# Kernel optimization log

Hardware: AMD Instinct MI355X
Metric: run time of the kernel (lower is better)

The kernel has to match this reference:

```python
import jax, jax.numpy as jnp
import numpy as np

DIM = 512
NUM_HEADS = 8
HEAD_DIM = DIM // NUM_HEADS
MAX_FRAMES = 64
EPS = 1e-5


def setup_inputs() -> dict:
    key = jax.random.key(0)
    ks = jax.random.split(key, 6)
    x = jax.random.normal(ks[0], (4, DIM, 16, 32, 32), dtype=jnp.float32)
    W_qkv = jax.random.normal(ks[1], (3 * DIM, DIM), dtype=jnp.float32) * (DIM ** -0.5)
    W_proj = jax.random.normal(ks[2], (DIM, DIM), dtype=jnp.float32) * (DIM ** -0.5)
    b_proj = jnp.zeros((DIM,), dtype=jnp.float32)
    rel_bias = jax.random.normal(ks[3], (MAX_FRAMES, MAX_FRAMES), dtype=jnp.float32) * 0.02
    ln_g = jnp.ones((DIM,), dtype=jnp.float32)
    ln_b = jnp.zeros((DIM,), dtype=jnp.float32)
    return {"x": x, "W_qkv": W_qkv, "W_proj": W_proj, "b_proj": b_proj,
            "rel_bias": rel_bias, "ln_g": ln_g, "ln_b": ln_b}


def reference(x, W_qkv, W_proj, b_proj, rel_bias, ln_g, ln_b):
    B, C, F, H, W = x.shape
    h = NUM_HEADS
    scale = HEAD_DIM ** -0.5
    # (B,C,F,H,W) -> (B*H*W, F, C)
    xr = jnp.transpose(x, (0, 3, 4, 2, 1)).reshape(B * H * W, F, C)
    residual = xr
    # LayerNorm over channel dim
    mu = jnp.mean(xr, axis=-1, keepdims=True)
    var = jnp.mean(jnp.square(xr - mu), axis=-1, keepdims=True)
    xn = (xr - mu) * jax.lax.rsqrt(var + EPS) * ln_g + ln_b
    # QKV projection (torch Linear: x @ W.T)
    qkv = xn @ W_qkv.T  # (BHW, F, 3C)
    q, k, v = jnp.split(qkv, 3, axis=-1)
    split_heads = lambda t: t.reshape(t.shape[0], F, h, HEAD_DIM).transpose(0, 2, 1, 3)
    q, k, v = split_heads(q), split_heads(k), split_heads(v)  # (BHW, h, F, d)
    attn = jnp.einsum('bhid,bhjd->bhij', q, k) * scale + rel_bias[:F, :F]
    attn = jax.nn.softmax(attn, axis=-1)
    out = jnp.einsum('bhij,bhjd->bhid', attn, v)  # (BHW, h, F, d)
    out = out.transpose(0, 2, 1, 3).reshape(B * H * W, F, C)
    out = out @ W_proj.T + b_proj + residual
    # (B*H*W, F, C) -> (B, C, F, H, W)
    out = out.reshape(B, H, W, F, C).transpose(0, 4, 3, 1, 2)
    return out
```

## Files before the change

### kernel.cpp

```cpp
#include <hip/hip_runtime.h>

typedef unsigned short ushort_t;
typedef __attribute__((ext_vector_type(4))) float f32x4;
typedef __attribute__((ext_vector_type(8))) short s16x8;
typedef __attribute__((ext_vector_type(4))) short s16x4;

#define SB 8388608
#define SC 16384
#define SF 1024

static __device__ __forceinline__ float bf2f(ushort_t u) {
    union { float f; unsigned int i; } x; x.i = ((unsigned int)u) << 16; return x.f;
}
static __device__ __forceinline__ ushort_t f2bf(float f) {
    union { float f; unsigned int i; } x; x.f = f;
    unsigned int u = x.i;
    unsigned int r = (u + 0x7FFFu + ((u >> 16) & 1u)) >> 16;
    return (ushort_t)r;
}

static __device__ __forceinline__ void gload16(const void* g, void* l) {
    __builtin_amdgcn_global_load_lds(
        (const __attribute__((address_space(1))) unsigned int*)g,
        (__attribute__((address_space(3))) unsigned int*)l, 16, 0, 0);
}

static __device__ __forceinline__ void wg_barrier() {
    asm volatile("" ::: "memory");
    __builtin_amdgcn_s_barrier();
    asm volatile("" ::: "memory");
}

__global__ void k_cvt(const float* __restrict__ a, int n1,
                      const float* __restrict__ b, int n2,
                      ushort_t* __restrict__ o1, ushort_t* __restrict__ o2) {
    int i = blockIdx.x * blockDim.x + threadIdx.x;
    if (i < n1) o1[i] = f2bf(a[i]);
    if (i < n2) o2[i] = f2bf(b[i]);
}

__global__ __launch_bounds__(256) void k_ln_transpose(
        const float* __restrict__ x, const float* __restrict__ g,
        const float* __restrict__ bta, ushort_t* __restrict__ xn) {
    __shared__ float tile[32 * 513];
    __shared__ float gg[512];
    __shared__ float bb[512];
    int bid = blockIdx.x;
    int b = bid >> 9;
    int f = (bid >> 5) & 15;
    int h = bid & 31;
    int t = threadIdx.x;
    for (int c = t; c < 512; c += 256) { gg[c] = g[c]; bb[c] = bta[c]; }
    const float* xp = x + (size_t)b * SB + (size_t)f * SF + h * 32;
    int wq4 = (t & 7) * 4;
    int c0 = t >> 3;
    for (int it = 0; it < 16; ++it) {
        int c = c0 + it * 32;
        f32x4 v = *(const f32x4*)(xp + (size_t)c * SC + wq4);
        tile[(wq4 + 0) * 513 + c] = v[0];
        tile[(wq4 + 1) * 513 + c] = v[1];
        tile[(wq4 + 2) * 513 + c] = v[2];
        tile[(wq4 + 3) * 513 + c] = v[3];
    }
    __syncthreads();
    int lane = t & 63;
    int wave = t >> 6;
    for (int wi = 0; wi < 8; ++wi) {
        int ww = wave * 8 + wi;
        float s = 0.f, s2 = 0.f;
        #pragma unroll
        for (int j = 0; j < 8; ++j) {
            float v = tile[ww * 513 + lane + j * 64];
            s += v; s2 += v * v;
        }
        #pragma unroll
        for (int off = 32; off; off >>= 1) { s += __shfl_xor(s, off); s2 += __shfl_xor(s2, off); }
        float mean = s * (1.f / 512.f);
        float var = s2 * (1.f / 512.f) - mean * mean;
        float rstd = rsqrtf(var + 1e-5f);
        size_t row = ((size_t)((b * 32 + h) * 32 + ww)) * 16 + f;
        ushort_t* op = xn + row * 512 + lane * 8;
        union { ushort_t a[8]; s16x8 v; } u;
        #pragma unroll
        for (int j = 0; j < 8; ++j) {
            int c = lane * 8 + j;
            float v = tile[ww * 513 + c];
            u.a[j] = f2bf((v - mean) * rstd * gg[c] + bb[c]);
        }
        *(s16x8*)op = u.v;
    }
}

__global__ __launch_bounds__(512) void k_qkv_attn(
        const ushort_t* __restrict__ xn, const ushort_t* __restrict__ wq,
        const float* __restrict__ rb, ushort_t* __restrict__ att) {
    __shared__ __align__(16) char U[122880];
    ushort_t* qsm = (ushort_t*)(U);
    ushort_t* ksm = (ushort_t*)(U + 16384);
    ushort_t* vT  = (ushort_t*)(U + 32768);

    const int t = threadIdx.x;
    const int lane = t & 63;
    const int wv = t >> 6;
    const int l16 = lane & 15;
    const int lg = lane >> 4;
    const int m0 = blockIdx.x * 128;
    const int wm = wv >> 2;
    const int wn = wv & 3;
    ushort_t* psw = ksm + wv * 1024;
    ushort_t* olw = qsm + wv * 1024;

    auto stageA = [&](int buf, int kb) {
        ushort_t* dst = (ushort_t*)(U + buf * 16384);
        #pragma unroll
        for (int it = 0; it < 2; ++it) {
            int f = t + it * 512;
            int row = f >> 3, slot = f & 7;
            const ushort_t* src = xn + (size_t)(m0 + row) * 512 + kb * 64 + ((slot ^ (row & 7)) << 3);
            gload16(src, dst + f * 8);
        }
    };
    auto stageB = [&](int buf, int kb, int h) {
        ushort_t* dst = (ushort_t*)(U + 49152 + buf * 24576);
        #pragma unroll
        for (int it = 0; it < 3; ++it) {
            int f = t + it * 512;
            int brow = f >> 3, slot = f & 7;
            int wrow = (brow >> 6) * 512 + h * 64 + (brow & 63);
            const ushort_t* src = wq + (size_t)wrow * 512 + kb * 64 + ((slot ^ (brow & 7)) << 3);
            gload16(src, dst + f * 8);
        }
    };

    for (int h = 0; h < 8; ++h) {
        __syncthreads();
        stageA(0, 0); stageB(0, 0, h);
        stageA(1, 1); stageB(1, 1, h);

        f32x4 acc[4][3];
        #pragma unroll
        for (int a1 = 0; a1 < 4; ++a1)
            #pragma unroll
            for (int a2 = 0; a2 < 3; ++a2)
                acc[a1][a2] = (f32x4){0.f, 0.f, 0.f, 0.f};

        for (int kb = 0; kb < 8; ++kb) {
            int cur = kb % 3;
            if (kb < 6) {
                stageA((kb + 2) % 3, kb + 2);
                stageB((kb + 2) % 3, kb + 2, h);
                asm volatile("s_waitcnt vmcnt(10)" ::: "memory");
            } else if (kb == 6) {
                asm volatile("s_waitcnt vmcnt(5)" ::: "memory");
            } else {
                asm volatile("s_waitcnt vmcnt(0)" ::: "memory");
            }
            wg_barrier();
            const ushort_t* Ac = (const ushort_t*)(U + cur * 16384);
            const ushort_t* Bc = (const ushort_t*)(U + 49152 + cur * 24576);
            #pragma unroll
            for (int kk = 0; kk < 2; ++kk) {
                int koff = kk * 64 + lg * 16;
                s16x8 af[4], bf[3];
                #pragma unroll
                for (int mf = 0; mf < 4; ++mf) {
                    int row = wm * 64 + mf * 16 + l16;
                    af[mf] = *(const s16x8*)&Ac[row * 64 + ((koff ^ ((row & 7) << 4)) >> 1)];
                }
                #pragma unroll
                for (int nf = 0; nf < 3; ++nf) {
                    int nrow = wn * 48 + nf * 16 + l16;
                    bf[nf] = *(const s16x8*)&Bc[nrow * 64 + ((koff ^ ((nrow & 7) << 4)) >> 1)];
                }
                #pragma unroll
                for (int mf = 0; mf < 4; ++mf)
                    #pragma unroll
                    for (int nf = 0; nf < 3; ++nf)
                        acc[mf][nf] = __builtin_amdgcn_mfma_f32_16x16x32_bf16(af[mf], bf[nf], acc[mf][nf], 0, 0, 0);
            }
            wg_barrier();
        }

        #pragma unroll
        for (int mf = 0; mf < 4; ++mf) {
            int mbase = wm * 64 + mf * 16 + lg * 4;
            #pragma unroll
            for (int nf = 0; nf < 3; ++nf) {
                int nn = wn * 48 + nf * 16 + l16;
                int seg = nn >> 6;
                int d = nn & 63;
                if (seg == 2) {
                    union { s16x4 v; ushort_t a[4]; } pk;
                    #pragma unroll
                    for (int r = 0; r < 4; ++r) pk.a[r] = f2bf(acc[mf][nf][r]);
                    *(s16x4*)&vT[d * 136 + mbase] = pk.v;
                } else {
                    ushort_t* dst = seg ? ksm : qsm;
                    #pragma unroll
                    for (int r = 0; r < 4; ++r) {
                        int m = mbase + r;
                        dst[m * 64 + (d ^ ((m & 7) << 3))] = f2bf(acc[mf][nf][r]);
                    }
                }
            }
        }
        __syncthreads();

        {
            int arow = wv * 16 + l16;
            int sw = (arow & 7) << 4;
            f32x4 sacc = (f32x4){0.f, 0.f, 0.f, 0.f};
            #pragma unroll
            for (int kk = 0; kk < 2; ++kk) {
                int off = kk * 64 + lg * 16;
                s16x8 ka = *(const s16x8*)&ksm[arow * 64 + ((off ^ sw) >> 1)];
                s16x8 qb = *(const s16x8*)&qsm[arow * 64 + ((off ^ sw) >> 1)];
                sacc = __builtin_amdgcn_mfma_f32_16x16x32_bf16(ka, qb, sacc, 0, 0, 0);
            }
            const float* rbp = rb + l16 * 64 + lg * 4;
            float p[4];
            float mx = -1e30f;
            #pragma unroll
            for (int r = 0; r < 4; ++r) {
                p[r] = sacc[r] * 0.125f + rbp[r];
                mx = fmaxf(mx, p[r]);
            }
            mx = fmaxf(mx, __shfl_xor(mx, 16));
            mx = fmaxf(mx, __shfl_xor(mx, 32));
            float sum = 0.f;
            #pragma unroll
            for (int r = 0; r < 4; ++r) { p[r] = __expf(p[r] - mx); sum += p[r]; }
            sum += __shfl_xor(sum, 16);
            sum += __shfl_xor(sum, 32);
            float inv = 1.f / sum;
            {
                union { s16x4 v; ushort_t a[4]; } pk;
                #pragma unroll
                for (int r = 0; r < 4; ++r) pk.a[r] = f2bf(p[r] * inv);
                *(s16x4*)&psw[l16 * 16 + lg * 4] = pk.v;
            }
            asm volatile("s_waitcnt lgkmcnt(0)" ::: "memory");
            s16x8 ap = (s16x8){0, 0, 0, 0, 0, 0, 0, 0};
            if (lg < 2) ap = *(const s16x8*)&psw[l16 * 16 + lg * 8];
            int jj = (lg < 2) ? lg * 8 : 0;
            f32x4 ov[4];
            #pragma unroll
            for (int ff = 0; ff < 4; ++ff) {
                int d = ff * 16 + l16;
                s16x8 bv = *(const s16x8*)&vT[d * 136 + wv * 16 + jj];
                ov[ff] = __builtin_amdgcn_mfma_f32_16x16x32_bf16(ap, bv, (f32x4){0.f, 0.f, 0.f, 0.f}, 0, 0, 0);
            }
            #pragma unroll
            for (int ff = 0; ff < 4; ++ff)
                #pragma unroll
                for (int r = 0; r < 4; ++r)
                    olw[(lg * 4 + r) * 64 + ff * 16 + l16] = f2bf(ov[ff][r]);
            asm volatile("s_waitcnt lgkmcnt(0)" ::: "memory");
            {
                int i2 = lane >> 2;
                int c2 = (lane & 3) * 16;
                s16x8 w0 = *(const s16x8*)&olw[i2 * 64 + c2];
                s16x8 w1 = *(const s16x8*)&olw[i2 * 64 + c2 + 8];
                ushort_t* op = att + (size_t)(m0 + wv * 16 + i2) * 512 + h * 64 + c2;
                *(s16x8*)op = w0;
                *(s16x8*)(op + 8) = w1;
            }
        }
    }
}

__global__ __launch_bounds__(512) void k_proj_out(
        const ushort_t* __restrict__ att, const ushort_t* __restrict__ wp,
        const float* __restrict__ bp, const float* __restrict__ x,
        float* __restrict__ out) {
    __shared__ __align__(16) char U[73728];
    int bid = blockIdx.x;
    int nh = bid & 1;
    int fq = (bid >> 1) & 3;
    int h = (bid >> 3) & 31;
    int b = bid >> 8;
    const int n0 = nh * 256;
    const int t = threadIdx.x;
    const int lane = t & 63;
    const int wv = t >> 6;
    const int l16 = lane & 15;
    const int lg = lane >> 4;
    const int wm = wv >> 2;
    const int wn = wv & 3;
    size_t attbase = ((size_t)(b * 32 + h) * 32) * 16 + fq * 4;

    auto stA = [&](int buf, int ks) {
        int row = t >> 2, slot = t & 3;
        int w = row & 31, fl = row >> 5;
        const ushort_t* src = att + (attbase + (size_t)w * 16 + fl) * 512 + ks * 32 + ((slot ^ ((row >> 2) & 3)) << 3);
        gload16(src, (ushort_t*)(U + buf * 8192) + t * 8);
    };
    auto stB = [&](int buf, int ks) {
        #pragma unroll
        for (int i = 0; i < 2; ++i) {
            int u = t + i * 512;
            int row = u >> 2, slot = u & 3;
            const ushort_t* src = wp + (size_t)(n0 + row) * 512 + ks * 32 + ((slot ^ ((row >> 2) & 3)) << 3);
            gload16(src, (ushort_t*)(U + 24576 + buf * 16384) + u * 8);
        }
    };

    f32x4 acc[4][4];
    #pragma unroll
    for (int m = 0; m < 4; ++m)
        #pragma unroll
        for (int n = 0; n < 4; ++n)
            acc[m][n] = (f32x4){0.f, 0.f, 0.f, 0.f};

    stA(0, 0); stB(0, 0);
    stA(1, 1); stB(1, 1);
    for (int ks = 0; ks < 16; ++ks) {
        int cur = ks % 3;
        if (ks < 14) {
            stA((ks + 2) % 3, ks + 2);
            stB((ks + 2) % 3, ks + 2);
            asm volatile("s_waitcnt vmcnt(6)" ::: "memory");
        } else if (ks == 14) {
            asm volatile("s_waitcnt vmcnt(3)" ::: "memory");
        } else {
            asm volatile("s_waitcnt vmcnt(0)" ::: "memory");
        }
        wg_barrier();
        s16x8 af[4], bf[4];
        #pragma unroll
        for (int mf = 0; mf < 4; ++mf) {
            int row = wm * 64 + mf * 16 + l16;
            af[mf] = *(const s16x8*)((ushort_t*)(U + cur * 8192) + row * 32 + ((lg ^ ((row >> 2) & 3)) << 3));
        }
        #pragma unroll
        for (int nf = 0; nf < 4; ++nf) {
            int nrow = wn * 64 + nf * 16 + l16;
            bf[nf] = *(const s16x8*)((ushort_t*)(U + 24576 + cur * 16384) + nrow * 32 + ((lg ^ ((nrow >> 2) & 3)) << 3));
        }
        #pragma unroll
        for (int mf = 0; mf < 4; ++mf)
            #pragma unroll
            for (int nf = 0; nf < 4; ++nf)
                acc[mf][nf] = __builtin_amdgcn_mfma_f32_16x16x32_bf16(bf[nf], af[mf], acc[mf][nf], 0, 0, 0);
        wg_barrier();
    }

    size_t obase = (size_t)b * SB + (size_t)(fq * 4) * SF + h * 32;
    #pragma unroll
    for (int mf = 0; mf < 4; ++mf) {
        int m = wm * 64 + mf * 16 + l16;
        int w = m & 31, fl = m >> 5;
        size_t base_m = obase + (size_t)fl * SF + w;
        #pragma unroll
        for (int nf = 0; nf < 4; ++nf) {
            int col0 = n0 + wn * 64 + nf * 16 + lg * 4;
            #pragma unroll
            for (int r = 0; r < 4; ++r) {
                int col = col0 + r;
                size_t a = base_m + (size_t)col * SC;
                out[a] = acc[mf][nf][r] + bp[col] + x[a];
            }
        }
    }
}

extern "C" void kernel_launch(void* const* d_in, const int* in_sizes, int n_in,
                              void* d_out, int out_size, void* d_ws, size_t ws_size,
                              hipStream_t stream) {
    const float* x     = (const float*)d_in[0];
    const float* wqkv  = (const float*)d_in[1];
    const float* wproj = (const float*)d_in[2];
    const float* bproj = (const float*)d_in[3];
    const float* rb    = (const float*)d_in[4];
    const float* lng   = (const float*)d_in[5];
    const float* lnb   = (const float*)d_in[6];
    float* out = (float*)d_out;
    char* ws = (char*)d_ws;
    ushort_t* xn   = (ushort_t*)(ws);
    ushort_t* att  = (ushort_t*)(ws + 67108864);
    ushort_t* wq16 = (ushort_t*)(ws + 134217728);
    ushort_t* wp16 = (ushort_t*)(ws + 135790592);

    k_cvt<<<3072, 256, 0, stream>>>(wqkv, 1536 * 512, wproj, 512 * 512, wq16, wp16);
    k_ln_transpose<<<2048, 256, 0, stream>>>(x, lng, lnb, xn);
    k_qkv_attn<<<512, 512, 0, stream>>>(xn, wq16, rb, att);
    k_proj_out<<<1024, 512, 0, stream>>>(att, wp16, bproj, x, out);
}
```

Before: 320.3 us.

## Process two heads per QKV GEMM pass with double-buffered staging

The fused QKV+attention kernel now computes Q/K/V for two heads at once, a 384-wide N tile per pass. This halves how often the activation A-tile is reloaded and halves the number of head-loop iterations and barriers. The staging pipeline goes from triple to double buffering to fit the larger B tile, and each wave's accumulator count doubles to 24 f32x4 fragments. This raises register pressure and LDS use to 128KB, and the shallower prefetch may expose more global-load latency.

```diff
diff --git a/kernel.cpp b/kernel.cpp
--- a/kernel.cpp
+++ b/kernel.cpp
@@ -94,10 +94,7 @@
 __global__ __launch_bounds__(512) void k_qkv_attn(
         const ushort_t* __restrict__ xn, const ushort_t* __restrict__ wq,
         const float* __restrict__ rb, ushort_t* __restrict__ att) {
-    __shared__ __align__(16) char U[122880];
-    ushort_t* qsm = (ushort_t*)(U);
-    ushort_t* ksm = (ushort_t*)(U + 16384);
-    ushort_t* vT  = (ushort_t*)(U + 32768);
+    __shared__ __align__(16) char U[131072];
 
     const int t = threadIdx.x;
     const int lane = t & 63;
@@ -107,8 +104,8 @@
     const int m0 = blockIdx.x * 128;
     const int wm = wv >> 2;
     const int wn = wv & 3;
-    ushort_t* psw = ksm + wv * 1024;
-    ushort_t* olw = qsm + wv * 1024;
+    ushort_t* psw = (ushort_t*)(U + 100352) + wv * 256;
+    ushort_t* olw = (ushort_t*)(U + 104448) + wv * 1024;
 
     auto stageA = [&](int buf, int kb) {
         ushort_t* dst = (ushort_t*)(U + buf * 16384);
@@ -120,62 +117,62 @@
             gload16(src, dst + f * 8);
         }
     };
-    auto stageB = [&](int buf, int kb, int h) {
-        ushort_t* dst = (ushort_t*)(U + 49152 + buf * 24576);
-        #pragma unroll
-        for (int it = 0; it < 3; ++it) {
+    auto stageB = [&](int buf, int kb, int hp) {
+        ushort_t* dst = (ushort_t*)(U + 32768 + buf * 49152);
+        #pragma unroll
+        for (int it = 0; it < 6; ++it) {
             int f = t + it * 512;
             int brow = f >> 3, slot = f & 7;
-            int wrow = (brow >> 6) * 512 + h * 64 + (brow & 63);
+            int seg = brow >> 7;
+            int hh = (brow >> 6) & 1;
+            int d = brow & 63;
+            int wrow = seg * 512 + (hp * 2 + hh) * 64 + d;
             const ushort_t* src = wq + (size_t)wrow * 512 + kb * 64 + ((slot ^ (brow & 7)) << 3);
             gload16(src, dst + f * 8);
         }
     };
 
-    for (int h = 0; h < 8; ++h) {
+    for (int hp = 0; hp < 4; ++hp) {
         __syncthreads();
-        stageA(0, 0); stageB(0, 0, h);
-        stageA(1, 1); stageB(1, 1, h);
-
-        f32x4 acc[4][3];
+        stageA(0, 0); stageB(0, 0, hp);
+
+        f32x4 acc[4][6];
         #pragma unroll
         for (int a1 = 0; a1 < 4; ++a1)
             #pragma unroll
-            for (int a2 = 0; a2 < 3; ++a2)
+            for (int a2 = 0; a2 < 6; ++a2)
                 acc[a1][a2] = (f32x4){0.f, 0.f, 0.f, 0.f};
 
         for (int kb = 0; kb < 8; ++kb) {
-            int cur = kb % 3;
-            if (kb < 6) {
-                stageA((kb + 2) % 3, kb + 2);
-                stageB((kb + 2) % 3, kb + 2, h);
-                asm volatile("s_waitcnt vmcnt(10)" ::: "memory");
-            } else if (kb == 6) {
-                asm volatile("s_waitcnt vmcnt(5)" ::: "memory");
+            int cur = kb & 1;
+            if (kb < 7) {
+                stageA(cur ^ 1, kb + 1);
+                stageB(cur ^ 1, kb + 1, hp);
+                asm volatile("s_waitcnt vmcnt(8)" ::: "memory");
             } else {
                 asm volatile("s_waitcnt vmcnt(0)" ::: "memory");
             }
             wg_barrier();
             const ushort_t* Ac = (const ushort_t*)(U + cur * 16384);
-            const ushort_t* Bc = (const ushort_t*)(U + 49152 + cur * 24576);
+            const ushort_t* Bc = (const ushort_t*)(U + 32768 + cur * 49152);
             #pragma unroll
             for (int kk = 0; kk < 2; ++kk) {
                 int koff = kk * 64 + lg * 16;
-                s16x8 af[4], bf[3];
+                s16x8 af[4], bf[6];
                 #pragma unroll
                 for (int mf = 0; mf < 4; ++mf) {
                     int row = wm * 64 + mf * 16 + l16;
                     af[mf] = *(const s16x8*)&Ac[row * 64 + ((koff ^ ((row & 7) << 4)) >> 1)];
                 }
                 #pragma unroll
-                for (int nf = 0; nf < 3; ++nf) {
-                    int nrow = wn * 48 + nf * 16 + l16;
+                for (int nf = 0; nf < 6; ++nf) {
+                    int nrow = wn * 96 + nf * 16 + l16;
                     bf[nf] = *(const s16x8*)&Bc[nrow * 64 + ((koff ^ ((nrow & 7) << 4)) >> 1)];
                 }
                 #pragma unroll
                 for (int mf = 0; mf < 4; ++mf)
                     #pragma unroll
-                    for (int nf = 0; nf < 3; ++nf)
+                    for (int nf = 0; nf < 6; ++nf)
                         acc[mf][nf] = __builtin_amdgcn_mfma_f32_16x16x32_bf16(af[mf], bf[nf], acc[mf][nf], 0, 0, 0);
             }
             wg_barrier();
@@ -185,17 +182,19 @@
         for (int mf = 0; mf < 4; ++mf) {
             int mbase = wm * 64 + mf * 16 + lg * 4;
             #pragma unroll
-            for (int nf = 0; nf < 3; ++nf) {
-                int nn = wn * 48 + nf * 16 + l16;
-                int seg = nn >> 6;
+            for (int nf = 0; nf < 6; ++nf) {
+                int nn = wn * 96 + nf * 16 + l16;
+                int seg = nn >> 7;
+                int hh = (nn >> 6) & 1;
                 int d = nn & 63;
                 if (seg == 2) {
+                    ushort_t* vTh = (ushort_t*)(U + 65536 + hh * 17408);
                     union { s16x4 v; ushort_t a[4]; } pk;
                     #pragma unroll
                     for (int r = 0; r < 4; ++r) pk.a[r] = f2bf(acc[mf][nf][r]);
-                    *(s16x4*)&vT[d * 136 + mbase] = pk.v;
+                    *(s16x4*)&vTh[d * 136 + mbase] = pk.v;
                 } else {
-                    ushort_t* dst = seg ? ksm : qsm;
+                    ushort_t* dst = (ushort_t*)(U + (seg ? 32768 : 0) + hh * 16384);
                     #pragma unroll
                     for (int r = 0; r < 4; ++r) {
                         int m = mbase + r;
@@ -206,15 +205,20 @@
         }
         __syncthreads();
 
-        {
+        #pragma unroll
+        for (int pp = 0; pp < 2; ++pp) {
+            const ushort_t* qsmP = (const ushort_t*)(U + pp * 16384);
+            const ushort_t* ksmP = (const ushort_t*)(U + 32768 + pp * 16384);
+            const ushort_t* vTP  = (const ushort_t*)(U + 65536 + pp * 17408);
+            int hd = hp * 2 + pp;
             int arow = wv * 16 + l16;
             int sw = (arow & 7) << 4;
             f32x4 sacc = (f32x4){0.f, 0.f, 0.f, 0.f};
             #pragma unroll
             for (int kk = 0; kk < 2; ++kk) {
                 int off = kk * 64 + lg * 16;
-                s16x8 ka = *(const s16x8*)&ksm[arow * 64 + ((off ^ sw) >> 1)];
-                s16x8 qb = *(const s16x8*)&qsm[arow * 64 + ((off ^ sw) >> 1)];
+                s16x8 ka = *(const s16x8*)&ksmP[arow * 64 + ((off ^ sw) >> 1)];
+                s16x8 qb = *(const s16x8*)&qsmP[arow * 64 + ((off ^ sw) >> 1)];
                 sacc = __builtin_amdgcn_mfma_f32_16x16x32_bf16(ka, qb, sacc, 0, 0, 0);
             }
             const float* rbp = rb + l16 * 64 + lg * 4;
@@ -247,7 +251,7 @@
             #pragma unroll
             for (int ff = 0; ff < 4; ++ff) {
                 int d = ff * 16 + l16;
-                s16x8 bv = *(const s16x8*)&vT[d * 136 + wv * 16 + jj];
+                s16x8 bv = *(const s16x8*)&vTP[d * 136 + wv * 16 + jj];
                 ov[ff] = __builtin_amdgcn_mfma_f32_16x16x32_bf16(ap, bv, (f32x4){0.f, 0.f, 0.f, 0.f}, 0, 0, 0);
             }
             #pragma unroll
@@ -261,7 +265,7 @@
                 int c2 = (lane & 3) * 16;
                 s16x8 w0 = *(const s16x8*)&olw[i2 * 64 + c2];
                 s16x8 w1 = *(const s16x8*)&olw[i2 * 64 + c2 + 8];
-                ushort_t* op = att + (size_t)(m0 + wv * 16 + i2) * 512 + h * 64 + c2;
+                ushort_t* op = att + (size_t)(m0 + wv * 16 + i2) * 512 + hd * 64 + c2;
                 *(s16x8*)op = w0;
                 *(s16x8*)(op + 8) = w1;
             }
```

After: 490.1 us. 1.53x slower.

## Shrink QKV-attention blocks to 64 rows with 256 threads for two blocks per CU

Applied to the files above, without the earlier changes.

The fused QKV-projection and attention kernel now processes 64 rows per block with 4 waves instead of 128 rows with 8 waves. Each wave covers all 64 rows against its own 48-column slice of the head's q/k/v weights. The triple-buffered global-to-LDS pipeline with explicit vmcnt waits becomes a double buffer guarded by plain __syncthreads, and the LDS footprint drops to 64KB so two blocks can share a CU. The intent is better latency hiding across blocks, but the weight tiles are now reloaded for half as many rows, and the full barriers likely wait on the just-issued prefetch, which removes much of the load/compute overlap. k_proj_out also gets a min-blocks-per-CU launch bound.

```diff
diff --git a/kernel.cpp b/kernel.cpp
--- a/kernel.cpp
+++ b/kernel.cpp
@@ -91,42 +91,41 @@
     }
 }
 
-__global__ __launch_bounds__(512) void k_qkv_attn(
+__global__ __launch_bounds__(256, 2) void k_qkv_attn(
         const ushort_t* __restrict__ xn, const ushort_t* __restrict__ wq,
         const float* __restrict__ rb, ushort_t* __restrict__ att) {
-    __shared__ __align__(16) char U[122880];
-    ushort_t* qsm = (ushort_t*)(U);
-    ushort_t* ksm = (ushort_t*)(U + 16384);
-    ushort_t* vT  = (ushort_t*)(U + 32768);
+    __shared__ __align__(16) char U[65536];
 
     const int t = threadIdx.x;
     const int lane = t & 63;
     const int wv = t >> 6;
     const int l16 = lane & 15;
     const int lg = lane >> 4;
-    const int m0 = blockIdx.x * 128;
-    const int wm = wv >> 2;
-    const int wn = wv & 3;
-    ushort_t* psw = ksm + wv * 1024;
-    ushort_t* olw = qsm + wv * 1024;
+    const int m0 = blockIdx.x * 64;
+    ushort_t* qsm = (ushort_t*)(U);
+    ushort_t* ksm = (ushort_t*)(U + 8192);
+    ushort_t* vT  = (ushort_t*)(U + 16384);
+    ushort_t* psw = (ushort_t*)(U + 25600) + wv * 256;
+    ushort_t* olw = (ushort_t*)(U + 27648) + wv * 1024;
 
     auto stageA = [&](int buf, int kb) {
-        ushort_t* dst = (ushort_t*)(U + buf * 16384);
+        ushort_t* dst = (ushort_t*)(U + buf * 8192);
         #pragma unroll
         for (int it = 0; it < 2; ++it) {
-            int f = t + it * 512;
+            int f = t + it * 256;
             int row = f >> 3, slot = f & 7;
             const ushort_t* src = xn + (size_t)(m0 + row) * 512 + kb * 64 + ((slot ^ (row & 7)) << 3);
             gload16(src, dst + f * 8);
         }
     };
     auto stageB = [&](int buf, int kb, int h) {
-        ushort_t* dst = (ushort_t*)(U + 49152 + buf * 24576);
-        #pragma unroll
-        for (int it = 0; it < 3; ++it) {
-            int f = t + it * 512;
+        ushort_t* dst = (ushort_t*)(U + 16384 + buf * 24576);
+        #pragma unroll
+        for (int it = 0; it < 6; ++it) {
+            int f = t + it * 256;
             int brow = f >> 3, slot = f & 7;
-            int wrow = (brow >> 6) * 512 + h * 64 + (brow & 63);
+            int seg = brow >> 6;
+            int wrow = seg * 512 + h * 64 + (brow & 63);
             const ushort_t* src = wq + (size_t)wrow * 512 + kb * 64 + ((slot ^ (brow & 7)) << 3);
             gload16(src, dst + f * 8);
         }
@@ -135,7 +134,6 @@
     for (int h = 0; h < 8; ++h) {
         __syncthreads();
         stageA(0, 0); stageB(0, 0, h);
-        stageA(1, 1); stageB(1, 1, h);
 
         f32x4 acc[4][3];
         #pragma unroll
@@ -145,31 +143,23 @@
                 acc[a1][a2] = (f32x4){0.f, 0.f, 0.f, 0.f};
 
         for (int kb = 0; kb < 8; ++kb) {
-            int cur = kb % 3;
-            if (kb < 6) {
-                stageA((kb + 2) % 3, kb + 2);
-                stageB((kb + 2) % 3, kb + 2, h);
-                asm volatile("s_waitcnt vmcnt(10)" ::: "memory");
-            } else if (kb == 6) {
-                asm volatile("s_waitcnt vmcnt(5)" ::: "memory");
-            } else {
-                asm volatile("s_waitcnt vmcnt(0)" ::: "memory");
-            }
-            wg_barrier();
-            const ushort_t* Ac = (const ushort_t*)(U + cur * 16384);
-            const ushort_t* Bc = (const ushort_t*)(U + 49152 + cur * 24576);
+            int cur = kb & 1;
+            if (kb < 7) { stageA(cur ^ 1, kb + 1); stageB(cur ^ 1, kb + 1, h); }
+            __syncthreads();
+            const ushort_t* Ac = (const ushort_t*)(U + cur * 8192);
+            const ushort_t* Bc = (const ushort_t*)(U + 16384 + cur * 24576);
             #pragma unroll
             for (int kk = 0; kk < 2; ++kk) {
                 int koff = kk * 64 + lg * 16;
                 s16x8 af[4], bf[3];
                 #pragma unroll
                 for (int mf = 0; mf < 4; ++mf) {
-                    int row = wm * 64 + mf * 16 + l16;
+                    int row = mf * 16 + l16;
                     af[mf] = *(const s16x8*)&Ac[row * 64 + ((koff ^ ((row & 7) << 4)) >> 1)];
                 }
                 #pragma unroll
                 for (int nf = 0; nf < 3; ++nf) {
-                    int nrow = wn * 48 + nf * 16 + l16;
+                    int nrow = wv * 48 + nf * 16 + l16;
                     bf[nf] = *(const s16x8*)&Bc[nrow * 64 + ((koff ^ ((nrow & 7) << 4)) >> 1)];
                 }
                 #pragma unroll
@@ -178,22 +168,22 @@
                     for (int nf = 0; nf < 3; ++nf)
                         acc[mf][nf] = __builtin_amdgcn_mfma_f32_16x16x32_bf16(af[mf], bf[nf], acc[mf][nf], 0, 0, 0);
             }
-            wg_barrier();
+            __syncthreads();
         }
 
         #pragma unroll
         for (int mf = 0; mf < 4; ++mf) {
-            int mbase = wm * 64 + mf * 16 + lg * 4;
+            int mbase = mf * 16 + lg * 4;
             #pragma unroll
             for (int nf = 0; nf < 3; ++nf) {
-                int nn = wn * 48 + nf * 16 + l16;
+                int nn = wv * 48 + nf * 16 + l16;
                 int seg = nn >> 6;
                 int d = nn & 63;
                 if (seg == 2) {
                     union { s16x4 v; ushort_t a[4]; } pk;
                     #pragma unroll
                     for (int r = 0; r < 4; ++r) pk.a[r] = f2bf(acc[mf][nf][r]);
-                    *(s16x4*)&vT[d * 136 + mbase] = pk.v;
+                    *(s16x4*)&vT[d * 72 + mbase] = pk.v;
                 } else {
                     ushort_t* dst = seg ? ksm : qsm;
                     #pragma unroll
@@ -239,7 +229,7 @@
                 for (int r = 0; r < 4; ++r) pk.a[r] = f2bf(p[r] * inv);
                 *(s16x4*)&psw[l16 * 16 + lg * 4] = pk.v;
             }
-            asm volatile("s_waitcnt lgkmcnt(0)" ::: "memory");
+            __syncthreads();
             s16x8 ap = (s16x8){0, 0, 0, 0, 0, 0, 0, 0};
             if (lg < 2) ap = *(const s16x8*)&psw[l16 * 16 + lg * 8];
             int jj = (lg < 2) ? lg * 8 : 0;
@@ -247,7 +237,7 @@
             #pragma unroll
             for (int ff = 0; ff < 4; ++ff) {
                 int d = ff * 16 + l16;
-                s16x8 bv = *(const s16x8*)&vT[d * 136 + wv * 16 + jj];
+                s16x8 bv = *(const s16x8*)&vT[d * 72 + wv * 16 + jj];
                 ov[ff] = __builtin_amdgcn_mfma_f32_16x16x32_bf16(ap, bv, (f32x4){0.f, 0.f, 0.f, 0.f}, 0, 0, 0);
             }
             #pragma unroll
@@ -255,7 +245,7 @@
                 #pragma unroll
                 for (int r = 0; r < 4; ++r)
                     olw[(lg * 4 + r) * 64 + ff * 16 + l16] = f2bf(ov[ff][r]);
-            asm volatile("s_waitcnt lgkmcnt(0)" ::: "memory");
+            __syncthreads();
             {
                 int i2 = lane >> 2;
                 int c2 = (lane & 3) * 16;
@@ -269,7 +259,7 @@
     }
 }
 
-__global__ __launch_bounds__(512) void k_proj_out(
+__global__ __launch_bounds__(512, 2) void k_proj_out(
         const ushort_t* __restrict__ att, const ushort_t* __restrict__ wp,
         const float* __restrict__ bp, const float* __restrict__ x,
         float* __restrict__ out) {
@@ -383,6 +373,6 @@
 
     k_cvt<<<3072, 256, 0, stream>>>(wqkv, 1536 * 512, wproj, 512 * 512, wq16, wp16);
     k_ln_transpose<<<2048, 256, 0, stream>>>(x, lng, lnb, xn);
-    k_qkv_attn<<<512, 512, 0, stream>>>(xn, wq16, rb, att);
+    k_qkv_attn<<<1024, 256, 0, stream>>>(xn, wq16, rb, att);
     k_proj_out<<<1024, 512, 0, stream>>>(att, wp16, bproj, x, out);
 }
```

New measurement: 333.5 us. +4.1%, slower.
